# Kernel tuning notes

Measured on AMD Instinct MI355X. Metric: run time of the kernel, lower is better.

Reference implementation:

```python
import jax, jax.numpy as jnp
import numpy as np

A_NUM = 9
C_NUM = 20


def generate_anchor(anc, grid):
    # anc: (A,2) w,h ; grid: (B,H,W,2) centers -> anchors (B,A,H,W,4)
    centers = grid[:, None]                      # (B,1,H,W,2)
    half = anc.reshape(1, -1, 1, 1, 2) * 0.5     # (1,A,1,1,2)
    return jnp.concatenate([centers - half, centers + half], axis=-1)


def iou_matrix(proposals, bboxes):
    # proposals: (B,A,H,W,4) -> (B,K,4); bboxes: (B,N,5)
    B = proposals.shape[0]
    p = proposals.reshape(B, -1, 4)[:, :, None, :]   # (B,K,1,4)
    bb = bboxes[:, None, :, :]                       # (B,1,N,5)
    s_p = (p[..., 2] - p[..., 0]) * (p[..., 3] - p[..., 1])
    s_b = (bb[..., 2] - bb[..., 0]) * (bb[..., 3] - bb[..., 1])
    ix1 = jnp.maximum(p[..., 0], bb[..., 0])
    iy1 = jnp.maximum(p[..., 1], bb[..., 1])
    ix2 = jnp.minimum(p[..., 2], bb[..., 2])
    iy2 = jnp.minimum(p[..., 3], bb[..., 3])
    s_i = jnp.clip(ix2 - ix1, 0.0) * jnp.clip(iy2 - iy1, 0.0)
    s_u = s_p + s_b - s_i
    iou = jnp.clip(s_i / (s_u + 1e-8), 0.0)
    invalid = (s_u <= 0) | (s_p <= 0) | (s_b <= 0) | (bb[..., 0] < 0)
    return jnp.where(invalid, 0.0, iou)              # (B,K,N)


def extract_anchor_data(anchor_data, idx):
    # anchor_data: (B,A,D,H,W) -> flat (B*A*H*W, D) -> gather
    B, A, D, H, W = anchor_data.shape
    flat = jnp.transpose(anchor_data, (0, 1, 3, 4, 2)).reshape(-1, D)
    return flat[idx]


def extract_class_scores(all_scores, idx, num_anchors):
    # all_scores: (B,C,H,W) -> (B,A,H,W,C) flat -> gather
    B, C, H, W = all_scores.shape
    s = jnp.transpose(all_scores, (0, 2, 3, 1))[:, None]          # (B,1,H,W,C)
    s = jnp.broadcast_to(s, (B, num_anchors, H, W, C)).reshape(-1, C)
    return s[idx]


def setup_inputs() -> dict:
    key = jax.random.key(0)
    ks = jax.random.split(key, 8)
    B, Cin, H, W = 32, 1280, 28, 28
    N, M = 64, 4096
    hid, out_ch = 128, 5 * A_NUM + C_NUM
    features = jax.random.normal(ks[0], (B, Cin, H, W), dtype=jnp.float32)
    # grid of feature-cell centers (GenerateGrid-style)
    xs = jnp.arange(W, dtype=jnp.float32) + 0.5
    ys = jnp.arange(H, dtype=jnp.float32) + 0.5
    gx, gy = jnp.meshgrid(xs, ys, indexing='xy')
    grid = jnp.broadcast_to(jnp.stack([gx, gy], axis=-1), (B, H, W, 2))
    anc = jnp.array([[1.0, 1], [2, 2], [3, 3], [4, 4], [5, 5], [2, 3], [3, 2], [3, 5], [5, 3]], dtype=jnp.float32)
    tl = jax.random.uniform(ks[1], (B, N, 2), minval=0.0, maxval=20.0)
    wh = jax.random.uniform(ks[2], (B, N, 2), minval=1.0, maxval=8.0)
    cls = jax.random.randint(ks[3], (B, N, 1), 0, C_NUM).astype(jnp.float32)
    bb = jnp.concatenate([tl, tl + wh, cls], axis=-1)
    valid = jax.random.uniform(ks[4], (B, N, 1)) > 0.25
    bboxes = jnp.where(valid, bb, -1.0)
    K = B * A_NUM * H * W
    pos_anchor_idx = jax.random.randint(ks[5], (M,), 0, K, dtype=jnp.int64 if jax.config.jax_enable_x64 else jnp.int32)
    neg_anchor_idx = jax.random.randint(ks[6], (M,), 0, K, dtype=pos_anchor_idx.dtype)
    W1 = jax.random.normal(ks[7], (hid, Cin), dtype=jnp.float32) * 0.02
    b1 = jnp.zeros((hid,), dtype=jnp.float32)
    W2 = jax.random.normal(jax.random.fold_in(key, 99), (out_ch, hid), dtype=jnp.float32) * 0.02
    b2 = jnp.zeros((out_ch,), dtype=jnp.float32)
    return {"features": features, "grid": grid, "anc": anc, "bboxes": bboxes,
            "pos_anchor_idx": pos_anchor_idx, "neg_anchor_idx": neg_anchor_idx,
            "W1": W1, "b1": b1, "W2": W2, "b2": b2}


def reference(features, grid, anc, bboxes, pos_anchor_idx, neg_anchor_idx, W1, b1, W2, b2):
    B, Cin, H, W = features.shape
    A, C = A_NUM, C_NUM
    # anchors + broadcast IoU matrix
    anchors = generate_anchor(anc, grid)                 # (B,A,H,W,4)
    iou_mat = iou_matrix(anchors, bboxes)                # (B,A*H*W,N)
    # prediction head: 1x1 conv -> (dropout eval: identity) -> leaky_relu -> 1x1 conv
    h = jnp.einsum('bchw,oc->bohw', features, W1) + b1[None, :, None, None]
    h = jax.nn.leaky_relu(h, negative_slope=0.01)
    out = jnp.einsum('bchw,oc->bohw', h, W2) + b2[None, :, None, None]  # (B,5A+C,H,W)
    anchor_raw = out[:, :5 * A].reshape(B, A, 5, H, W)
    conf_sq = jax.nn.sigmoid(anchor_raw[:, :, 0:1])      # (B,A,1,H,W)
    off_raw = anchor_raw[:, :, 1:]                       # (B,A,4,H,W)
    off_sq = jnp.concatenate([jax.nn.sigmoid(off_raw[:, :, :2]) - 0.5, off_raw[:, :, 2:]], axis=2)
    class_raw = out[:, 5 * A:]                           # (B,C,H,W)
    # training path: irregular gathers
    class_scores = extract_class_scores(class_raw, pos_anchor_idx, A)   # (M,C)
    offsets = extract_anchor_data(off_sq, pos_anchor_idx)               # (M,4)
    conf_pos = extract_anchor_data(conf_sq, pos_anchor_idx)             # (M,1)
    conf_neg = extract_anchor_data(conf_sq, neg_anchor_idx)             # (M,1)
    conf_scores = jnp.concatenate([conf_pos, conf_neg], axis=0)         # (2M,1)
    return conf_scores, offsets, class_scores, iou_mat
```

## Files before the change

kernel.cpp:

```cpp
#include <hip/hip_runtime.h>
#include <cstdint>

#define A_NUM 9
#define C_NUM 20
#define B_SZ 32
#define HW 784
#define P_NUM (A_NUM*HW)
#define NBOX 64
#define CIN 1280
#define HID 128
#define M_IDX 4096
#define NK 40
#define ASTR 40

#define CONF_OFF 0
#define OFFS_OFF (2*M_IDX)
#define CLS_OFF  (OFFS_OFF + 4*M_IDX)
#define IOU_OFF  (CLS_OFF + C_NUM*M_IDX)

typedef short bf16x8 __attribute__((ext_vector_type(8)));
typedef float f32x4  __attribute__((ext_vector_type(4)));

__device__ __forceinline__ unsigned pack_bf16(float lo, float hi) {
  unsigned a = __builtin_bit_cast(unsigned, lo);
  unsigned b = __builtin_bit_cast(unsigned, hi);
  return ((a + 0x8000u) >> 16) | ((b + 0x8000u) & 0xffff0000u);
}

__global__ __launch_bounds__(256) void prep_w1(const float* __restrict__ W1,
                                               unsigned* __restrict__ W1sw) {
  int id = blockIdx.x * 256 + threadIdx.x;
  int kk = (id & 3) * 8;
  int n  = (id >> 2) & 127;
  int ks = id >> 9;
  const float* src = W1 + n * CIN + ks * 32 + kk;
  float4 x = *(const float4*)src;
  float4 y = *(const float4*)(src + 4);
  uint4 p;
  p.x = pack_bf16(x.x, x.y);
  p.y = pack_bf16(x.z, x.w);
  p.z = pack_bf16(y.x, y.y);
  p.w = pack_bf16(y.z, y.w);
  *(uint4*)&W1sw[(ks * 4096 + n * 32 + kk) >> 1] = p;
}

__global__ __launch_bounds__(256) void gemm1_mfma(
    const float* __restrict__ F, const unsigned short* __restrict__ W1sw,
    const float* __restrict__ b1, float* __restrict__ Hws) {
  __shared__ unsigned short Asm[2][128 * ASTR];
  __shared__ unsigned short Bsm[2][128 * 32];

  const int b = blockIdx.y;
  const int m0 = blockIdx.x * 128;
  const int t = threadIdx.x;
  const int wave = t >> 6, lane = t & 63;
  const int wm = wave >> 1, wn = wave & 1;
  const int quad = lane >> 4, lo = lane & 15;

  const int sm = t & 127;
  const int kh = t >> 7;
  const int gm = m0 + sm;
  const bool mval = gm < HW;
  const float* Fb = F + (size_t)b * CIN * HW + (mval ? gm : 0);

  f32x4 acc[4][4];
#pragma unroll
  for (int i = 0; i < 4; i++)
#pragma unroll
    for (int j = 0; j < 4; j++) acc[i][j] = (f32x4){0.f, 0.f, 0.f, 0.f};

  float va[16];
  uint4 vb0, vb1;

  auto loadG = [&](int ks) {
    const int k0 = ks * 32 + kh * 16;
#pragma unroll
    for (int i = 0; i < 16; i++) va[i] = Fb[(size_t)(k0 + i) * HW];
    const unsigned short* g = W1sw + ks * 4096 + t * 16;
    vb0 = *(const uint4*)g;
    vb1 = *(const uint4*)(g + 8);
  };

  auto stage = [&](int buf) {
    uint4 p0, p1;
    if (mval) {
      p0.x = pack_bf16(va[0], va[1]);   p0.y = pack_bf16(va[2], va[3]);
      p0.z = pack_bf16(va[4], va[5]);   p0.w = pack_bf16(va[6], va[7]);
      p1.x = pack_bf16(va[8], va[9]);   p1.y = pack_bf16(va[10], va[11]);
      p1.z = pack_bf16(va[12], va[13]); p1.w = pack_bf16(va[14], va[15]);
    } else {
      p0 = (uint4){0, 0, 0, 0}; p1 = p0;
    }
    *(uint4*)&Asm[buf][sm * ASTR + kh * 16] = p0;
    *(uint4*)&Asm[buf][sm * ASTR + kh * 16 + 8] = p1;
    *(uint4*)&Bsm[buf][t * 16] = vb0;
    *(uint4*)&Bsm[buf][t * 16 + 8] = vb1;
  };

  auto compute = [&](int buf) {
    const unsigned short* Ab = &Asm[buf][(wm * 64 + lo) * ASTR + quad * 8];
    const unsigned short* Bb = &Bsm[buf][(wn * 64 + lo) * 32 + quad * 8];
    bf16x8 af[4], bfr[4];
#pragma unroll
    for (int i = 0; i < 4; i++) af[i] = *(const bf16x8*)(Ab + i * 16 * ASTR);
#pragma unroll
    for (int j = 0; j < 4; j++) bfr[j] = *(const bf16x8*)(Bb + j * 16 * 32);
#pragma unroll
    for (int i = 0; i < 4; i++)
#pragma unroll
      for (int j = 0; j < 4; j++)
        acc[i][j] = __builtin_amdgcn_mfma_f32_16x16x32_bf16(af[i], bfr[j],
                                                            acc[i][j], 0, 0, 0);
  };

  loadG(0);
  stage(0);
  __syncthreads();
  for (int ks = 0; ks < NK; ks++) {
    const int cur = ks & 1;
    if (ks + 1 < NK) loadG(ks + 1);
    compute(cur);
    if (ks + 1 < NK) stage(cur ^ 1);
    __syncthreads();
  }

#pragma unroll
  for (int i = 0; i < 4; i++) {
    const int mbase = m0 + wm * 64 + i * 16 + quad * 4;
#pragma unroll
    for (int j = 0; j < 4; j++) {
      const int n = wn * 64 + j * 16 + lo;
      const float bias = b1[n];
#pragma unroll
      for (int r = 0; r < 4; r++) {
        const int mm = mbase + r;
        if (mm < HW) {
          float v = acc[i][j][r] + bias;
          Hws[((size_t)(b * HW + mm)) * HID + n] = v > 0.f ? v : 0.01f * v;
        }
      }
    }
  }
}

__global__ __launch_bounds__(256) void iou_kernel(
    const float* __restrict__ grid, const float* __restrict__ anc,
    const float* __restrict__ bboxes, float* __restrict__ out) {
  __shared__ float sb[NBOX * 5];
  int b = blockIdx.y;
  int t = threadIdx.x;
  for (int i = t; i < NBOX * 5; i += 256) sb[i] = bboxes[b * NBOX * 5 + i];
  __syncthreads();
  int p = blockIdx.x * 4 + (t >> 6);
  int n = t & 63;
  int a = p / HW;
  int hw = p - a * HW;
  float cx = grid[(b * HW + hw) * 2 + 0];
  float cy = grid[(b * HW + hw) * 2 + 1];
  float hx = anc[a * 2 + 0] * 0.5f, hy = anc[a * 2 + 1] * 0.5f;
  float x1 = cx - hx, y1 = cy - hy, x2 = cx + hx, y2 = cy + hy;
  float sp = (x2 - x1) * (y2 - y1);
  float bx1 = sb[n * 5 + 0], by1 = sb[n * 5 + 1];
  float bx2 = sb[n * 5 + 2], by2 = sb[n * 5 + 3];
  float s_b = (bx2 - bx1) * (by2 - by1);
  float ix1 = fmaxf(x1, bx1), iy1 = fmaxf(y1, by1);
  float ix2 = fminf(x2, bx2), iy2 = fminf(y2, by2);
  float si = fmaxf(ix2 - ix1, 0.f) * fmaxf(iy2 - iy1, 0.f);
  float su = sp + s_b - si;
  float iou = fmaxf(si / (su + 1e-8f), 0.f);
  bool invalid = (su <= 0.f) | (sp <= 0.f) | (s_b <= 0.f) | (bx1 < 0.f);
  out[((size_t)(b * P_NUM + p)) * 64 + n] = invalid ? 0.f : iou;
}

__global__ __launch_bounds__(64) void gather_kernel(
    const int* __restrict__ pos_idx, const int* __restrict__ neg_idx,
    const float* __restrict__ Hws, const float* __restrict__ W2,
    const float* __restrict__ b2, float* __restrict__ out) {
  __shared__ float sh[HID];
  int blk = blockIdx.x;
  int l = threadIdx.x;
  bool pos = blk < M_IDX;
  int idx = pos ? pos_idx[blk] : neg_idx[blk - M_IDX];
  int b = idx / P_NUM;
  int r = idx - b * P_NUM;
  int a = r / HW;
  int hw = r - a * HW;
  const float* hrow = Hws + ((size_t)(b * HW + hw)) * HID;
  float v0 = hrow[2 * l], v1 = hrow[2 * l + 1];
  sh[2 * l] = v0; sh[2 * l + 1] = v1;
  __syncthreads();
  if (pos) {
    if (l < 25) {
      int o = (l < 5) ? (a * 5 + l) : (5 * A_NUM + (l - 5));
      const float* w = W2 + o * HID;
      float dot = b2[o];
#pragma unroll 8
      for (int k = 0; k < HID; k++) dot = fmaf(w[k], sh[k], dot);
      if (l == 0) {
        out[CONF_OFF + blk] = 1.f / (1.f + expf(-dot));
      } else if (l < 3) {
        out[OFFS_OFF + blk * 4 + (l - 1)] = 1.f / (1.f + expf(-dot)) - 0.5f;
      } else if (l < 5) {
        out[OFFS_OFF + blk * 4 + (l - 1)] = dot;
      } else {
        out[CLS_OFF + blk * C_NUM + (l - 5)] = dot;
      }
    }
  } else {
    int o = a * 5;
    const float* w = W2 + o * HID;
    float part = fmaf(w[2 * l], v0, w[2 * l + 1] * v1);
#pragma unroll
    for (int off = 32; off > 0; off >>= 1) part += __shfl_down(part, off);
    if (l == 0) out[CONF_OFF + blk] = 1.f / (1.f + expf(-(b2[o] + part)));
  }
}

extern "C" void kernel_launch(void* const* d_in, const int* in_sizes, int n_in,
                              void* d_out, int out_size, void* d_ws, size_t ws_size,
                              hipStream_t stream) {
  const float* features = (const float*)d_in[0];
  const float* grid     = (const float*)d_in[1];
  const float* anc      = (const float*)d_in[2];
  const float* bboxes   = (const float*)d_in[3];
  const int*   pos_idx  = (const int*)d_in[4];
  const int*   neg_idx  = (const int*)d_in[5];
  const float* W1       = (const float*)d_in[6];
  const float* b1       = (const float*)d_in[7];
  const float* W2       = (const float*)d_in[8];
  const float* b2       = (const float*)d_in[9];
  float* out = (float*)d_out;

  unsigned* W1sw = (unsigned*)d_ws;
  float* Hws = (float*)((char*)d_ws + 327680);

  hipLaunchKernelGGL(prep_w1, dim3(80), dim3(256), 0, stream, W1, W1sw);
  hipLaunchKernelGGL(gemm1_mfma, dim3(7, B_SZ), dim3(256), 0, stream,
                     features, (const unsigned short*)W1sw, b1, Hws);
  hipLaunchKernelGGL(iou_kernel, dim3(P_NUM / 4, B_SZ), dim3(256),
                     0, stream, grid, anc, bboxes, out + IOU_OFF);
  hipLaunchKernelGGL(gather_kernel, dim3(2 * M_IDX), dim3(64),
                     0, stream, pos_idx, neg_idx, Hws, W2, b2, out);
}
```

Baseline: 289.5 us.

## Split-K the first GEMM and fuse bias/activation reduction into gather

```diff
diff --git a/kernel.cpp b/kernel.cpp
--- a/kernel.cpp
+++ b/kernel.cpp
@@ -10,8 +10,10 @@
 #define CIN 1280
 #define HID 128
 #define M_IDX 4096
-#define NK 40
+#define KSPLIT 4
+#define KS_PER 10
 #define ASTR 40
+#define PSTR ((size_t)B_SZ * HW * HID)
 
 #define CONF_OFF 0
 #define OFFS_OFF (2*M_IDX)
@@ -28,12 +30,15 @@
 }
 
 __global__ __launch_bounds__(256) void prep_w1(const float* __restrict__ W1,
-                                               unsigned* __restrict__ W1sw) {
+                                               uint4* __restrict__ W1f) {
   int id = blockIdx.x * 256 + threadIdx.x;
-  int kk = (id & 3) * 8;
-  int n  = (id >> 2) & 127;
+  int lane = id & 63;
+  int ntile = (id >> 6) & 7;
   int ks = id >> 9;
-  const float* src = W1 + n * CIN + ks * 32 + kk;
+  int lo = lane & 15, quad = lane >> 4;
+  int n = ntile * 16 + lo;
+  int k0 = ks * 32 + quad * 8;
+  const float* src = W1 + n * CIN + k0;
   float4 x = *(const float4*)src;
   float4 y = *(const float4*)(src + 4);
   uint4 p;
@@ -41,103 +46,100 @@
   p.y = pack_bf16(x.z, x.w);
   p.z = pack_bf16(y.x, y.y);
   p.w = pack_bf16(y.z, y.w);
-  *(uint4*)&W1sw[(ks * 4096 + n * 32 + kk) >> 1] = p;
+  W1f[id] = p;
 }
 
 __global__ __launch_bounds__(256) void gemm1_mfma(
-    const float* __restrict__ F, const unsigned short* __restrict__ W1sw,
-    const float* __restrict__ b1, float* __restrict__ Hws) {
-  __shared__ unsigned short Asm[2][128 * ASTR];
-  __shared__ unsigned short Bsm[2][128 * 32];
+    const float* __restrict__ F, const unsigned short* __restrict__ W1f,
+    float* __restrict__ Part) {
+  __shared__ unsigned short Asm[2][64 * ASTR];
 
   const int b = blockIdx.y;
-  const int m0 = blockIdx.x * 128;
+  const int z = blockIdx.z;
+  const int m0 = blockIdx.x * 64;
   const int t = threadIdx.x;
   const int wave = t >> 6, lane = t & 63;
-  const int wm = wave >> 1, wn = wave & 1;
   const int quad = lane >> 4, lo = lane & 15;
-
-  const int sm = t & 127;
-  const int kh = t >> 7;
+  const int ksbase = z * KS_PER;
+
+  const int sm = t & 63;
+  const int kh = t >> 6;
   const int gm = m0 + sm;
   const bool mval = gm < HW;
   const float* Fb = F + (size_t)b * CIN * HW + (mval ? gm : 0);
 
-  f32x4 acc[4][4];
+  f32x4 acc[4][2];
 #pragma unroll
   for (int i = 0; i < 4; i++)
 #pragma unroll
-    for (int j = 0; j < 4; j++) acc[i][j] = (f32x4){0.f, 0.f, 0.f, 0.f};
-
-  float va[16];
-  uint4 vb0, vb1;
-
-  auto loadG = [&](int ks) {
-    const int k0 = ks * 32 + kh * 16;
-#pragma unroll
-    for (int i = 0; i < 16; i++) va[i] = Fb[(size_t)(k0 + i) * HW];
-    const unsigned short* g = W1sw + ks * 4096 + t * 16;
-    vb0 = *(const uint4*)g;
-    vb1 = *(const uint4*)(g + 8);
-  };
-
-  auto stage = [&](int buf) {
-    uint4 p0, p1;
+    for (int j = 0; j < 2; j++) acc[i][j] = (f32x4){0.f, 0.f, 0.f, 0.f};
+
+  float va[8];
+  uint4 vb[2][2];
+
+  auto loadA = [&](int kk) {
+    const int k0 = (ksbase + kk) * 32 + kh * 8;
+#pragma unroll
+    for (int i = 0; i < 8; i++) va[i] = Fb[(size_t)(k0 + i) * HW];
+  };
+  auto loadB = [&](int kk, uint4* dst) {
+    const unsigned short* g =
+        W1f + (size_t)(((ksbase + kk) * 8 + wave * 2) * 64 + lane) * 8;
+    dst[0] = *(const uint4*)g;
+    dst[1] = *(const uint4*)(g + 512);
+  };
+  auto stageA = [&](int buf) {
+    uint4 p;
     if (mval) {
-      p0.x = pack_bf16(va[0], va[1]);   p0.y = pack_bf16(va[2], va[3]);
-      p0.z = pack_bf16(va[4], va[5]);   p0.w = pack_bf16(va[6], va[7]);
-      p1.x = pack_bf16(va[8], va[9]);   p1.y = pack_bf16(va[10], va[11]);
-      p1.z = pack_bf16(va[12], va[13]); p1.w = pack_bf16(va[14], va[15]);
+      p.x = pack_bf16(va[0], va[1]);
+      p.y = pack_bf16(va[2], va[3]);
+      p.z = pack_bf16(va[4], va[5]);
+      p.w = pack_bf16(va[6], va[7]);
     } else {
-      p0 = (uint4){0, 0, 0, 0}; p1 = p0;
-    }
-    *(uint4*)&Asm[buf][sm * ASTR + kh * 16] = p0;
-    *(uint4*)&Asm[buf][sm * ASTR + kh * 16 + 8] = p1;
-    *(uint4*)&Bsm[buf][t * 16] = vb0;
-    *(uint4*)&Bsm[buf][t * 16 + 8] = vb1;
-  };
-
-  auto compute = [&](int buf) {
-    const unsigned short* Ab = &Asm[buf][(wm * 64 + lo) * ASTR + quad * 8];
-    const unsigned short* Bb = &Bsm[buf][(wn * 64 + lo) * 32 + quad * 8];
-    bf16x8 af[4], bfr[4];
+      p = (uint4){0, 0, 0, 0};
+    }
+    *(uint4*)&Asm[buf][sm * ASTR + kh * 8] = p;
+  };
+  auto compute = [&](int buf, uint4* bv) {
+    const unsigned short* Ab = &Asm[buf][lo * ASTR + quad * 8];
+    bf16x8 af[4];
 #pragma unroll
     for (int i = 0; i < 4; i++) af[i] = *(const bf16x8*)(Ab + i * 16 * ASTR);
-#pragma unroll
-    for (int j = 0; j < 4; j++) bfr[j] = *(const bf16x8*)(Bb + j * 16 * 32);
-#pragma unroll
-    for (int i = 0; i < 4; i++)
-#pragma unroll
-      for (int j = 0; j < 4; j++)
-        acc[i][j] = __builtin_amdgcn_mfma_f32_16x16x32_bf16(af[i], bfr[j],
-                                                            acc[i][j], 0, 0, 0);
-  };
-
-  loadG(0);
-  stage(0);
+    bf16x8 b0 = __builtin_bit_cast(bf16x8, bv[0]);
+    bf16x8 b1 = __builtin_bit_cast(bf16x8, bv[1]);
+#pragma unroll
+    for (int i = 0; i < 4; i++) {
+      acc[i][0] = __builtin_amdgcn_mfma_f32_16x16x32_bf16(af[i], b0, acc[i][0], 0, 0, 0);
+      acc[i][1] = __builtin_amdgcn_mfma_f32_16x16x32_bf16(af[i], b1, acc[i][1], 0, 0, 0);
+    }
+  };
+
+  loadA(0);
+  loadB(0, vb[0]);
+  stageA(0);
   __syncthreads();
-  for (int ks = 0; ks < NK; ks++) {
-    const int cur = ks & 1;
-    if (ks + 1 < NK) loadG(ks + 1);
-    compute(cur);
-    if (ks + 1 < NK) stage(cur ^ 1);
+  for (int kk = 0; kk < KS_PER; kk++) {
+    const int cur = kk & 1;
+    if (kk + 1 < KS_PER) {
+      loadA(kk + 1);
+      loadB(kk + 1, vb[cur ^ 1]);
+    }
+    compute(cur, vb[cur]);
+    if (kk + 1 < KS_PER) stageA(cur ^ 1);
     __syncthreads();
   }
 
+  float* Pz = Part + ((size_t)(z * B_SZ + b) * HW) * HID;
 #pragma unroll
   for (int i = 0; i < 4; i++) {
-    const int mbase = m0 + wm * 64 + i * 16 + quad * 4;
-#pragma unroll
-    for (int j = 0; j < 4; j++) {
-      const int n = wn * 64 + j * 16 + lo;
-      const float bias = b1[n];
+    const int mbase = m0 + i * 16 + quad * 4;
+#pragma unroll
+    for (int j = 0; j < 2; j++) {
+      const int n = wave * 32 + j * 16 + lo;
 #pragma unroll
       for (int r = 0; r < 4; r++) {
         const int mm = mbase + r;
-        if (mm < HW) {
-          float v = acc[i][j][r] + bias;
-          Hws[((size_t)(b * HW + mm)) * HID + n] = v > 0.f ? v : 0.01f * v;
-        }
+        if (mm < HW) Pz[(size_t)mm * HID + n] = acc[i][j][r];
       }
     }
   }
@@ -174,8 +176,9 @@
 
 __global__ __launch_bounds__(64) void gather_kernel(
     const int* __restrict__ pos_idx, const int* __restrict__ neg_idx,
-    const float* __restrict__ Hws, const float* __restrict__ W2,
-    const float* __restrict__ b2, float* __restrict__ out) {
+    const float* __restrict__ Part, const float* __restrict__ b1,
+    const float* __restrict__ W2, const float* __restrict__ b2,
+    float* __restrict__ out) {
   __shared__ float sh[HID];
   int blk = blockIdx.x;
   int l = threadIdx.x;
@@ -185,8 +188,15 @@
   int r = idx - b * P_NUM;
   int a = r / HW;
   int hw = r - a * HW;
-  const float* hrow = Hws + ((size_t)(b * HW + hw)) * HID;
-  float v0 = hrow[2 * l], v1 = hrow[2 * l + 1];
+  const float2* row = (const float2*)(Part + ((size_t)(b * HW + hw)) * HID) + l;
+  float2 s0 = row[0];
+  float2 s1 = row[PSTR / 2];
+  float2 s2 = row[2 * (PSTR / 2)];
+  float2 s3 = row[3 * (PSTR / 2)];
+  float v0 = s0.x + s1.x + s2.x + s3.x + b1[2 * l];
+  float v1 = s0.y + s1.y + s2.y + s3.y + b1[2 * l + 1];
+  v0 = v0 > 0.f ? v0 : 0.01f * v0;
+  v1 = v1 > 0.f ? v1 : 0.01f * v1;
   sh[2 * l] = v0; sh[2 * l + 1] = v1;
   __syncthreads();
   if (pos) {
@@ -231,14 +241,14 @@
   const float* b2       = (const float*)d_in[9];
   float* out = (float*)d_out;
 
-  unsigned* W1sw = (unsigned*)d_ws;
-  float* Hws = (float*)((char*)d_ws + 327680);
-
-  hipLaunchKernelGGL(prep_w1, dim3(80), dim3(256), 0, stream, W1, W1sw);
-  hipLaunchKernelGGL(gemm1_mfma, dim3(7, B_SZ), dim3(256), 0, stream,
-                     features, (const unsigned short*)W1sw, b1, Hws);
+  uint4* W1f = (uint4*)d_ws;
+  float* Part = (float*)((char*)d_ws + 327680);
+
+  hipLaunchKernelGGL(prep_w1, dim3(80), dim3(256), 0, stream, W1, W1f);
+  hipLaunchKernelGGL(gemm1_mfma, dim3(13, B_SZ, KSPLIT), dim3(256), 0, stream,
+                     features, (const unsigned short*)W1f, Part);
   hipLaunchKernelGGL(iou_kernel, dim3(P_NUM / 4, B_SZ), dim3(256),
                      0, stream, grid, anc, bboxes, out + IOU_OFF);
   hipLaunchKernelGGL(gather_kernel, dim3(2 * M_IDX), dim3(64),
-                     0, stream, pos_idx, neg_idx, Hws, W2, b2, out);
-}
+                     0, stream, pos_idx, neg_idx, Part, b1, W2, b2, out);
+}
```

Result: no change. 287.7 us (-0.6%).
